# Performance work log

Hardware: AMD Instinct MI355X
Metric: run time of the kernel (lower is better)

## Reference

```python
import jax, jax.numpy as jnp
import numpy as np

N, C_IN, C_OUT, C_REL, T, V = 64, 256, 256, 32, 64, 25

def conv1x1(x, w, b):
    # x: (n, ci, a, b), w: (co, ci), b: (co,) -> (n, co, a, b)
    return jnp.einsum('oc,ncab->noab', w, x) + b[None, :, None, None]

def setup_inputs() -> dict:
    key = jax.random.key(0)
    ks = jax.random.split(key, 10)
    s_in = 1.0 / np.sqrt(C_IN)
    s_rel = 1.0 / np.sqrt(C_REL)
    return {
        'x': jax.random.normal(ks[0], (N, C_IN, T, V), dtype=jnp.float32),
        'A': jax.random.normal(ks[1], (V, V), dtype=jnp.float32),
        'w1': jax.random.uniform(ks[2], (C_REL, C_IN), jnp.float32, -s_in, s_in),
        'b1': jax.random.uniform(ks[3], (C_REL,), jnp.float32, -s_in, s_in),
        'w2': jax.random.uniform(ks[4], (C_REL, C_IN), jnp.float32, -s_in, s_in),
        'b2': jax.random.uniform(ks[5], (C_REL,), jnp.float32, -s_in, s_in),
        'w3': jax.random.uniform(ks[6], (C_OUT, C_IN), jnp.float32, -s_in, s_in),
        'b3': jax.random.uniform(ks[7], (C_OUT,), jnp.float32, -s_in, s_in),
        'w4': jax.random.uniform(ks[8], (C_OUT, C_REL), jnp.float32, -s_rel, s_rel),
        'b4': jax.random.uniform(ks[9], (C_OUT,), jnp.float32, -s_rel, s_rel),
        'threhold': 0,
        'alpha': 1,
    }

def reference(x, A, w1, b1, w2, b2, w3, b3, w4, b4, threhold, alpha):
    # x: (n, c, t, v)
    # pooled 1x1 convs: fold the T-mean before the channel mix (linear ops commute)
    xm = x.mean(-2)                                   # (n, c, v)
    x1 = jnp.einsum('oc,ncv->nov', w1, xm) + b1[None, :, None]   # (n, r, v)
    x2 = jnp.einsum('oc,ncv->nov', w2, xm) + b2[None, :, None]   # (n, r, v)
    x3 = conv1x1(x, w3, b3)                           # (n, co, t, v)
    # channel-wise affinity: outer difference + tanh -> (n, r, v, v)
    aff = jnp.tanh(x1[:, :, :, None] - x2[:, :, None, :])
    # 1x1 conv over rel channels, scale, add adjacency
    attn = jnp.einsum('or,nruv->nouv', w4, aff) + b4[None, :, None, None]
    attn = attn * alpha + A[None, None]               # (n, co, v, v)
    # graph conv contraction
    out = jnp.einsum('ncuv,nctu->nctv', attn, x3)     # (n, co, t, v)
    return out
```

## Files before the change

### kernel.cpp

```cpp
#include <hip/hip_runtime.h>

#define N_  64
#define CI  256
#define CO  256
#define CR  32
#define T_  64
#define V_  25
#define TV  (T_*V_)
#define VV  (V_*V_)
#define ATS 640

typedef __attribute__((ext_vector_type(8))) short bshort8;
typedef __attribute__((ext_vector_type(4))) float f32x4;

__device__ inline unsigned short f2bf(float f) {
    unsigned int u = __float_as_uint(f);
    return (unsigned short)((u + 0x7FFFu + ((u >> 16) & 1u)) >> 16);
}

__global__ __launch_bounds__(256) void k_mean_cvt(const float* __restrict__ x,
                                                  const float* __restrict__ w3,
                                                  const float* __restrict__ w4,
                                                  float* __restrict__ xm,
                                                  unsigned short* __restrict__ w3f,
                                                  unsigned short* __restrict__ w4f) {
    int b = blockIdx.x;
    if (b < 1600) {
        int idx = b * 256 + threadIdx.x;
        int v  = idx % V_;
        int nc = idx / V_;
        const float* p = x + (size_t)nc * TV + v;
        float s = 0.f;
        for (int t = 0; t < T_; ++t) s += p[t * V_];
        xm[idx] = s * (1.f / T_);
    } else if (b < 1632) {
        int f = (b - 1600) * 256 + threadIdx.x;
        int lane = f & 63;
        int ks = (f >> 6) & 7;
        int ot = f >> 9;
        const float* src = w3 + (size_t)(ot * 16 + (lane & 15)) * CI + ks * 32 + (lane >> 4) * 8;
        bshort8 v;
        #pragma unroll
        for (int i = 0; i < 8; ++i) v[i] = (short)f2bf(src[i]);
        *(bshort8*)(w3f + (size_t)f * 8) = v;
    } else {
        int f = (b - 1632) * 256 + threadIdx.x;
        int lane = f & 63;
        int ot = f >> 6;
        const float* src = w4 + (size_t)(ot * 16 + (lane & 15)) * CR + (lane >> 4) * 8;
        bshort8 v;
        #pragma unroll
        for (int i = 0; i < 8; ++i) v[i] = (short)f2bf(src[i]);
        *(bshort8*)(w4f + (size_t)f * 8) = v;
    }
}

__global__ __launch_bounds__(256) void k_x1x2(const float* __restrict__ xm,
                                              const float* __restrict__ w1,
                                              const float* __restrict__ b1,
                                              const float* __restrict__ w2,
                                              const float* __restrict__ b2,
                                              float* __restrict__ x1,
                                              float* __restrict__ x2) {
    int n = blockIdx.x, q = blockIdx.y;
    __shared__ float s_xm[CI * V_];
    const float4* src = (const float4*)(xm + (size_t)n * CI * V_);
    for (int i = threadIdx.x; i < CI * V_ / 4; i += 256) ((float4*)s_xm)[i] = src[i];
    __syncthreads();
    if (threadIdx.x < 200) {
        int idx = q * 200 + threadIdx.x;
        int r = idx / V_, v = idx % V_;
        const float* wr1 = w1 + (size_t)r * CI;
        const float* wr2 = w2 + (size_t)r * CI;
        float p1a = 0.f, p1b = 0.f, p2a = 0.f, p2b = 0.f;
        #pragma unroll 4
        for (int c = 0; c < CI; c += 2) {
            float xv0 = s_xm[c * V_ + v];
            float xv1 = s_xm[(c + 1) * V_ + v];
            p1a += wr1[c] * xv0;  p1b += wr1[c + 1] * xv1;
            p2a += wr2[c] * xv0;  p2b += wr2[c + 1] * xv1;
        }
        x1[n * CR * V_ + idx] = p1a + p1b + b1[r];
        x2[n * CR * V_ + idx] = p2a + p2b + b2[r];
    }
}

__global__ __launch_bounds__(256) void k_attn(const float* __restrict__ x1,
                                              const float* __restrict__ x2,
                                              const unsigned short* __restrict__ w4f,
                                              const float* __restrict__ b4,
                                              const float* __restrict__ A,
                                              const int* __restrict__ alpha_p,
                                              unsigned short* __restrict__ attnT) {
    int n = blockIdx.x;
    __shared__ float s_x1[CR * V_];
    __shared__ float s_x2[CR * V_];
    __shared__ float s_A[VV];
    int tid = threadIdx.x;
    float alpha = (float)alpha_p[0];
    for (int i = tid; i < CR * V_; i += 256) {
        s_x1[i] = x1[n * CR * V_ + i];
        s_x2[i] = x2[n * CR * V_ + i];
    }
    for (int i = tid; i < VV; i += 256) s_A[i] = A[i];
    __syncthreads();
    int wave = tid >> 6, lane = tid & 63;
    int task = blockIdx.y * 4 + wave;
    int og   = task & 3;
    int ug   = task >> 2;
    int o0   = og * 64;
    int quad = lane >> 4, c16 = lane & 15;
    bshort8 a[4];
    #pragma unroll
    for (int ot = 0; ot < 4; ++ot)
        a[ot] = *(const bshort8*)(w4f + (size_t)(((og * 4) + ot) * 64 + lane) * 8);
    float4 bv[4];
    #pragma unroll
    for (int ot = 0; ot < 4; ++ot)
        bv[ot] = *(const float4*)(b4 + o0 + ot * 16 + quad * 4);
    int r0 = quad * 8;
    #pragma unroll
    for (int it = 0; it < 5; ++it) {
        int uv0 = (ug * 5 + it) * 16;
        int uvc = uv0 + c16;
        bool valid = uvc < VV;
        int uvcc = valid ? uvc : (VV - 1);
        int u = uvcc % V_, v = uvcc / V_;
        bshort8 b;
        #pragma unroll
        for (int i = 0; i < 8; ++i) {
            float d = s_x1[(r0 + i) * V_ + u] - s_x2[(r0 + i) * V_ + v];
            b[i] = (short)f2bf(tanhf(d));
        }
        float Auv = s_A[u * V_ + v];
        f32x4 acc[4];
        #pragma unroll
        for (int ot = 0; ot < 4; ++ot)
            acc[ot] = __builtin_amdgcn_mfma_f32_16x16x32_bf16(a[ot], b, (f32x4){0,0,0,0}, 0, 0, 0);
        if (valid) {
            #pragma unroll
            for (int ot = 0; ot < 4; ++ot) {
                #pragma unroll
                for (int r = 0; r < 4; ++r) {
                    int o = o0 + ot * 16 + quad * 4 + r;
                    float bval = (r == 0) ? bv[ot].x : (r == 1) ? bv[ot].y
                               : (r == 2) ? bv[ot].z : bv[ot].w;
                    attnT[(size_t)(n * CO + o) * ATS + uvc] =
                        f2bf((acc[ot][r] + bval) * alpha + Auv);
                }
            }
        }
    }
}

__global__ __launch_bounds__(256) void k_gemm1(const float* __restrict__ x,
                                               const unsigned short* __restrict__ w3f,
                                               const float* __restrict__ b3,
                                               unsigned short* __restrict__ x3) {
    int n = blockIdx.x, j0 = blockIdx.y * 64;
    __shared__ unsigned short sB[64 * 256];
    int tid  = threadIdx.x;
    int lane = tid & 63, wave = tid >> 6;
    const float* gx = x + (size_t)n * CI * TV + j0;
    for (int i = 0; i < 16; ++i) {
        int task = i * 256 + tid;
        int c = task >> 4, chunk = task & 15;
        float4 v = *(const float4*)(gx + (size_t)c * TV + chunk * 4);
        int g0 = c >> 3, cl = c & 7;
        #pragma unroll
        for (int k = 0; k < 4; ++k) {
            int j = chunk * 4 + k;
            int f = g0 ^ (j & 7) ^ ((j >> 2) & 7);
            float val = (k == 0) ? v.x : (k == 1) ? v.y : (k == 2) ? v.z : v.w;
            sB[j * 256 + f * 8 + cl] = f2bf(val);
        }
    }
    __syncthreads();
    int quad = lane >> 4, c16 = lane & 15;
    const bshort8* Af = (const bshort8*)w3f;
    f32x4 acc[4][4];
    #pragma unroll
    for (int mt = 0; mt < 4; ++mt)
        #pragma unroll
        for (int nt = 0; nt < 4; ++nt) acc[mt][nt] = (f32x4){0,0,0,0};
    #pragma unroll
    for (int ks = 0; ks < 8; ++ks) {
        bshort8 b[4], a[4];
        #pragma unroll
        for (int nt = 0; nt < 4; ++nt) {
            int rB = nt * 16 + c16;
            int cidx = ks * 4 + quad;
            int f = cidx ^ (rB & 7) ^ ((rB >> 2) & 7);
            b[nt] = *(const bshort8*)(&sB[rB * 256 + f * 8]);
        }
        #pragma unroll
        for (int mt = 0; mt < 4; ++mt)
            a[mt] = Af[(size_t)(((wave * 4 + mt) * 8 + ks) * 64) + lane];
        #pragma unroll
        for (int mt = 0; mt < 4; ++mt)
            #pragma unroll
            for (int nt = 0; nt < 4; ++nt)
                acc[mt][nt] = __builtin_amdgcn_mfma_f32_16x16x32_bf16(a[mt], b[nt], acc[mt][nt], 0, 0, 0);
    }
    __syncthreads();
    unsigned short* eS = sB;
    #pragma unroll
    for (int pass = 0; pass < 2; ++pass) {
        if ((wave >> 1) == pass) {
            #pragma unroll
            for (int mt = 0; mt < 4; ++mt) {
                int o = wave * 64 + mt * 16 + quad * 4;
                float4 bvv = *(const float4*)(b3 + o);
                int ol = (wave & 1) * 64 + mt * 16 + quad * 4;
                #pragma unroll
                for (int nt = 0; nt < 4; ++nt) {
                    int jc = nt * 16 + c16;
                    eS[(ol + 0) * 72 + jc] = f2bf(acc[mt][nt][0] + bvv.x);
                    eS[(ol + 1) * 72 + jc] = f2bf(acc[mt][nt][1] + bvv.y);
                    eS[(ol + 2) * 72 + jc] = f2bf(acc[mt][nt][2] + bvv.z);
                    eS[(ol + 3) * 72 + jc] = f2bf(acc[mt][nt][3] + bvv.w);
                }
            }
        }
        __syncthreads();
        #pragma unroll
        for (int i = 0; i < 4; ++i) {
            int task = i * 256 + tid;
            int orow = task >> 3, seg = task & 7;
            bshort8 vv = *(const bshort8*)&eS[orow * 72 + seg * 8];
            *(bshort8*)(x3 + (size_t)(n * CO + pass * 128 + orow) * TV + j0 + seg * 8) = vv;
        }
        __syncthreads();
    }
}

__global__ __launch_bounds__(256) void k_contract(const unsigned short* __restrict__ x3,
                                                  const unsigned short* __restrict__ attnT,
                                                  float* __restrict__ out) {
    int no0 = blockIdx.x * 4;
    __shared__ __align__(16) unsigned char smem[28672];
    unsigned short* sA = (unsigned short*)smem;
    unsigned short* sB = (unsigned short*)(smem + 16384);
    float*          sO = (float*)smem;
    int tid = threadIdx.x;
    #pragma unroll
    for (int i = 0; i < 7; ++i) {
        int task = i * 256 + tid;
        if (task < 1792) {
            int p = task / 448, rem = task % 448;
            sA[p * 2048 + (rem / 7) * 32 + 25 + rem % 7] = 0;
        }
    }
    {
        int task = tid;
        for (int i = 0; i < 3; ++i, task += 256)
            if (task < 700) {
                int p = task / 175, rem = task % 175;
                sB[p * 1024 + (rem / 7) * 32 + 25 + rem % 7] = 0;
            }
    }
    #pragma unroll
    for (int i = 0; i < 4; ++i) {
        int task = i * 256 + tid;
        if (task < 800) {
            int p = task / 200, e8 = task % 200;
            bshort8 vv = *(const bshort8*)(x3 + (size_t)(no0 + p) * TV + e8 * 8);
            #pragma unroll
            for (int k = 0; k < 8; ++k) {
                int j = e8 * 8 + k;
                int t = j / 25, u = j % 25;
                sA[p * 2048 + t * 32 + u] = (unsigned short)vv[k];
            }
        }
    }
    #pragma unroll
    for (int i = 0; i < 2; ++i) {
        int task = i * 256 + tid;
        if (task < 316) {
            int p = task / 79, e8 = task % 79;
            bshort8 vv = *(const bshort8*)(attnT + (size_t)(no0 + p) * ATS + e8 * 8);
            #pragma unroll
            for (int k = 0; k < 8; ++k) {
                int idx = e8 * 8 + k;
                if (idx < VV) {
                    int v = idx / 25, u = idx % 25;
                    sB[p * 1024 + v * 32 + u] = (unsigned short)vv[k];
                }
            }
        }
    }
    __syncthreads();
    int p = tid >> 6, lane = tid & 63;
    int quad = lane >> 4, c16 = lane & 15;
    const unsigned short* pA = sA + p * 2048;
    const unsigned short* pB = sB + p * 1024;
    bshort8 a[4], b[2];
    #pragma unroll
    for (int mt = 0; mt < 4; ++mt) a[mt] = *(const bshort8*)&pA[(mt * 16 + c16) * 32 + quad * 8];
    #pragma unroll
    for (int nt = 0; nt < 2; ++nt) b[nt] = *(const bshort8*)&pB[(nt * 16 + c16) * 32 + quad * 8];
    f32x4 acc[4][2];
    #pragma unroll
    for (int mt = 0; mt < 4; ++mt)
        #pragma unroll
        for (int nt = 0; nt < 2; ++nt)
            acc[mt][nt] = __builtin_amdgcn_mfma_f32_16x16x32_bf16(a[mt], b[nt], (f32x4){0,0,0,0}, 0, 0, 0);
    __syncthreads();
    float* pO = sO + p * 1792;
    #pragma unroll
    for (int mt = 0; mt < 4; ++mt)
        #pragma unroll
        for (int nt = 0; nt < 2; ++nt) {
            int v = nt * 16 + c16;
            if (v < V_) {
                #pragma unroll
                for (int r = 0; r < 4; ++r) {
                    int t = mt * 16 + quad * 4 + r;
                    pO[t * 28 + v] = acc[mt][nt][r];
                }
            }
        }
    __syncthreads();
    #pragma unroll
    for (int i = 0; i < 25; ++i) {
        int idx = i * 256 + tid;
        int p2 = idx / TV, rem = idx % TV;
        int t = rem / 25, v = rem % 25;
        out[(size_t)(no0 + p2) * TV + rem] = sO[p2 * 1792 + t * 28 + v];
    }
}

extern "C" void kernel_launch(void* const* d_in, const int* in_sizes, int n_in,
                              void* d_out, int out_size, void* d_ws, size_t ws_size,
                              hipStream_t stream) {
    const float* x  = (const float*)d_in[0];
    const float* A  = (const float*)d_in[1];
    const float* w1 = (const float*)d_in[2];
    const float* b1 = (const float*)d_in[3];
    const float* w2 = (const float*)d_in[4];
    const float* b2 = (const float*)d_in[5];
    const float* w3 = (const float*)d_in[6];
    const float* b3 = (const float*)d_in[7];
    const float* w4 = (const float*)d_in[8];
    const float* b4 = (const float*)d_in[9];
    const int* alpha_p = (const int*)d_in[11];
    float* out = (float*)d_out;

    float* ws = (float*)d_ws;
    float* xm = ws;
    float* x1 = ws + 409600;
    float* x2 = ws + 460800;
    unsigned short* attnT = (unsigned short*)(ws + 512000);
    unsigned short* w3f   = attnT + (size_t)16384 * ATS;
    unsigned short* w4f   = w3f + 65536;
    unsigned short* x3    = w4f + 16384;

    k_mean_cvt<<<1636, 256, 0, stream>>>(x, w3, w4, xm, w3f, w4f);
    k_x1x2<<<dim3(N_, 4), 256, 0, stream>>>(xm, w1, b1, w2, b2, x1, x2);
    k_attn<<<dim3(N_, 8), 256, 0, stream>>>(x1, x2, w4f, b4, A, alpha_p, attnT);
    k_gemm1<<<dim3(N_, 25), 256, 0, stream>>>(x, w3f, b3, x3);
    k_contract<<<4096, 256, 0, stream>>>(x3, attnT, out);
}
```

Measured before the change: 297.9 us.

## Merge attention and GEMM kernels, tile T-mean via LDS, write contract output directly

Three changes. The T-mean reduction now stages 16-channel tiles of x through shared memory with float4 loads instead of strided scalar loads per (n,c,v). The attention-build and x3 GEMM kernels are combined into one launch with block-index dispatch, which removes a launch and lets the small attention work overlap the GEMM. The contraction kernel drops its shared-memory staging and writes results straight to global memory, giving up coalescing in exchange for fewer barriers and less LDS. The fused kernel now uses 64KB of static LDS for every block, including the attention blocks, which may lower occupancy.

```diff
diff --git a/kernel.cpp b/kernel.cpp
--- a/kernel.cpp
+++ b/kernel.cpp
@@ -25,16 +25,43 @@
                                                   unsigned short* __restrict__ w3f,
                                                   unsigned short* __restrict__ w4f) {
     int b = blockIdx.x;
-    if (b < 1600) {
-        int idx = b * 256 + threadIdx.x;
-        int v  = idx % V_;
-        int nc = idx / V_;
-        const float* p = x + (size_t)nc * TV + v;
-        float s = 0.f;
-        for (int t = 0; t < T_; ++t) s += p[t * V_];
-        xm[idx] = s * (1.f / T_);
-    } else if (b < 1632) {
-        int f = (b - 1600) * 256 + threadIdx.x;
+    int tid = threadIdx.x;
+    if (b < 1024) {
+        __shared__ float L[16 * 400];
+        int n = b >> 4, c0 = (b & 15) * 16;
+        float a0 = 0.f, a1 = 0.f;
+        for (int ch = 0; ch < 4; ++ch) {
+            for (int i = 0; i < 7; ++i) {
+                int task = i * 256 + tid;
+                if (task < 1600) {
+                    int c = task / 100, f4 = task % 100;
+                    *(float4*)&L[c * 400 + f4 * 4] =
+                        *(const float4*)(x + (size_t)(n * CI + c0 + c) * TV + ch * 400 + f4 * 4);
+                }
+            }
+            __syncthreads();
+            {
+                int c = tid / 25, v = tid % 25;
+                float s = 0.f;
+                #pragma unroll
+                for (int tl = 0; tl < 16; ++tl) s += L[c * 400 + tl * 25 + v];
+                a0 += s;
+            }
+            if (tid < 144) {
+                int oi = tid + 256;
+                int c = oi / 25, v = oi % 25;
+                float s = 0.f;
+                #pragma unroll
+                for (int tl = 0; tl < 16; ++tl) s += L[c * 400 + tl * 25 + v];
+                a1 += s;
+            }
+            __syncthreads();
+        }
+        xm[(size_t)(n * CI + c0) * V_ + tid] = a0 * (1.f / T_);
+        if (tid < 144)
+            xm[(size_t)(n * CI + c0) * V_ + tid + 256] = a1 * (1.f / T_);
+    } else if (b < 1056) {
+        int f = (b - 1024) * 256 + tid;
         int lane = f & 63;
         int ks = (f >> 6) & 7;
         int ot = f >> 9;
@@ -44,7 +71,7 @@
         for (int i = 0; i < 8; ++i) v[i] = (short)f2bf(src[i]);
         *(bshort8*)(w3f + (size_t)f * 8) = v;
     } else {
-        int f = (b - 1632) * 256 + threadIdx.x;
+        int f = (b - 1056) * 256 + tid;
         int lane = f & 63;
         int ot = f >> 6;
         const float* src = w4 + (size_t)(ot * 16 + (lane & 15)) * CR + (lane >> 4) * 8;
@@ -85,152 +112,155 @@
     }
 }
 
-__global__ __launch_bounds__(256) void k_attn(const float* __restrict__ x1,
-                                              const float* __restrict__ x2,
-                                              const unsigned short* __restrict__ w4f,
-                                              const float* __restrict__ b4,
-                                              const float* __restrict__ A,
-                                              const int* __restrict__ alpha_p,
-                                              unsigned short* __restrict__ attnT) {
-    int n = blockIdx.x;
-    __shared__ float s_x1[CR * V_];
-    __shared__ float s_x2[CR * V_];
-    __shared__ float s_A[VV];
+__global__ __launch_bounds__(256) void k_attn_gemm(const float* __restrict__ x,
+                                                   const unsigned short* __restrict__ w3f,
+                                                   const float* __restrict__ b3,
+                                                   unsigned short* __restrict__ x3,
+                                                   const float* __restrict__ x1,
+                                                   const float* __restrict__ x2,
+                                                   const unsigned short* __restrict__ w4f,
+                                                   const float* __restrict__ b4,
+                                                   const float* __restrict__ A,
+                                                   const int* __restrict__ alpha_p,
+                                                   unsigned short* __restrict__ attnT) {
+    __shared__ __align__(16) unsigned char smem[65536];
     int tid = threadIdx.x;
-    float alpha = (float)alpha_p[0];
-    for (int i = tid; i < CR * V_; i += 256) {
-        s_x1[i] = x1[n * CR * V_ + i];
-        s_x2[i] = x2[n * CR * V_ + i];
-    }
-    for (int i = tid; i < VV; i += 256) s_A[i] = A[i];
-    __syncthreads();
-    int wave = tid >> 6, lane = tid & 63;
-    int task = blockIdx.y * 4 + wave;
-    int og   = task & 3;
-    int ug   = task >> 2;
-    int o0   = og * 64;
-    int quad = lane >> 4, c16 = lane & 15;
-    bshort8 a[4];
-    #pragma unroll
-    for (int ot = 0; ot < 4; ++ot)
-        a[ot] = *(const bshort8*)(w4f + (size_t)(((og * 4) + ot) * 64 + lane) * 8);
-    float4 bv[4];
-    #pragma unroll
-    for (int ot = 0; ot < 4; ++ot)
-        bv[ot] = *(const float4*)(b4 + o0 + ot * 16 + quad * 4);
-    int r0 = quad * 8;
-    #pragma unroll
-    for (int it = 0; it < 5; ++it) {
-        int uv0 = (ug * 5 + it) * 16;
-        int uvc = uv0 + c16;
-        bool valid = uvc < VV;
-        int uvcc = valid ? uvc : (VV - 1);
-        int u = uvcc % V_, v = uvcc / V_;
-        bshort8 b;
-        #pragma unroll
-        for (int i = 0; i < 8; ++i) {
-            float d = s_x1[(r0 + i) * V_ + u] - s_x2[(r0 + i) * V_ + v];
-            b[i] = (short)f2bf(tanhf(d));
-        }
-        float Auv = s_A[u * V_ + v];
-        f32x4 acc[4];
+    int bb  = blockIdx.x;
+    if (bb < 1600) {
+        unsigned short* sB = (unsigned short*)smem;
+        int n = bb / 25, j0 = (bb % 25) * 64;
+        int lane = tid & 63, wave = tid >> 6;
+        const float* gx = x + (size_t)n * CI * TV + j0;
+        for (int i = 0; i < 16; ++i) {
+            int task = i * 256 + tid;
+            int c = task >> 4, chunk = task & 15;
+            float4 v = *(const float4*)(gx + (size_t)c * TV + chunk * 4);
+            int g0 = c >> 3, cl = c & 7;
+            #pragma unroll
+            for (int k = 0; k < 4; ++k) {
+                int j = chunk * 4 + k;
+                int f = g0 ^ (j & 7) ^ ((j >> 2) & 7);
+                float val = (k == 0) ? v.x : (k == 1) ? v.y : (k == 2) ? v.z : v.w;
+                sB[j * 256 + f * 8 + cl] = f2bf(val);
+            }
+        }
+        __syncthreads();
+        int quad = lane >> 4, c16 = lane & 15;
+        const bshort8* Af = (const bshort8*)w3f;
+        f32x4 acc[4][4];
+        #pragma unroll
+        for (int mt = 0; mt < 4; ++mt)
+            #pragma unroll
+            for (int nt = 0; nt < 4; ++nt) acc[mt][nt] = (f32x4){0,0,0,0};
+        #pragma unroll
+        for (int ks = 0; ks < 8; ++ks) {
+            bshort8 b[4], a[4];
+            #pragma unroll
+            for (int nt = 0; nt < 4; ++nt) {
+                int rB = nt * 16 + c16;
+                int cidx = ks * 4 + quad;
+                int f = cidx ^ (rB & 7) ^ ((rB >> 2) & 7);
+                b[nt] = *(const bshort8*)(&sB[rB * 256 + f * 8]);
+            }
+            #pragma unroll
+            for (int mt = 0; mt < 4; ++mt)
+                a[mt] = Af[(size_t)(((wave * 4 + mt) * 8 + ks) * 64) + lane];
+            #pragma unroll
+            for (int mt = 0; mt < 4; ++mt)
+                #pragma unroll
+                for (int nt = 0; nt < 4; ++nt)
+                    acc[mt][nt] = __builtin_amdgcn_mfma_f32_16x16x32_bf16(a[mt], b[nt], acc[mt][nt], 0, 0, 0);
+        }
+        __syncthreads();
+        unsigned short* eS = sB;
+        #pragma unroll
+        for (int pass = 0; pass < 2; ++pass) {
+            if ((wave >> 1) == pass) {
+                #pragma unroll
+                for (int mt = 0; mt < 4; ++mt) {
+                    int o = wave * 64 + mt * 16 + quad * 4;
+                    float4 bvv = *(const float4*)(b3 + o);
+                    int ol = (wave & 1) * 64 + mt * 16 + quad * 4;
+                    #pragma unroll
+                    for (int nt = 0; nt < 4; ++nt) {
+                        int jc = nt * 16 + c16;
+                        eS[(ol + 0) * 72 + jc] = f2bf(acc[mt][nt][0] + bvv.x);
+                        eS[(ol + 1) * 72 + jc] = f2bf(acc[mt][nt][1] + bvv.y);
+                        eS[(ol + 2) * 72 + jc] = f2bf(acc[mt][nt][2] + bvv.z);
+                        eS[(ol + 3) * 72 + jc] = f2bf(acc[mt][nt][3] + bvv.w);
+                    }
+                }
+            }
+            __syncthreads();
+            #pragma unroll
+            for (int i = 0; i < 4; ++i) {
+                int task = i * 256 + tid;
+                int orow = task >> 3, seg = task & 7;
+                bshort8 vv = *(const bshort8*)&eS[orow * 72 + seg * 8];
+                *(bshort8*)(x3 + (size_t)(n * CO + pass * 128 + orow) * TV + j0 + seg * 8) = vv;
+            }
+            __syncthreads();
+        }
+    } else {
+        float* s_x1 = (float*)smem;
+        float* s_x2 = s_x1 + CR * V_;
+        float* s_A  = s_x2 + CR * V_;
+        int b2 = bb - 1600;
+        int n = b2 >> 3, by = b2 & 7;
+        float alpha = (float)alpha_p[0];
+        for (int i = tid; i < CR * V_; i += 256) {
+            s_x1[i] = x1[n * CR * V_ + i];
+            s_x2[i] = x2[n * CR * V_ + i];
+        }
+        for (int i = tid; i < VV; i += 256) s_A[i] = A[i];
+        __syncthreads();
+        int wave = tid >> 6, lane = tid & 63;
+        int task = by * 4 + wave;
+        int og   = task & 3;
+        int ug   = task >> 2;
+        int o0   = og * 64;
+        int quad = lane >> 4, c16 = lane & 15;
+        bshort8 a[4];
         #pragma unroll
         for (int ot = 0; ot < 4; ++ot)
-            acc[ot] = __builtin_amdgcn_mfma_f32_16x16x32_bf16(a[ot], b, (f32x4){0,0,0,0}, 0, 0, 0);
-        if (valid) {
-            #pragma unroll
-            for (int ot = 0; ot < 4; ++ot) {
-                #pragma unroll
-                for (int r = 0; r < 4; ++r) {
-                    int o = o0 + ot * 16 + quad * 4 + r;
-                    float bval = (r == 0) ? bv[ot].x : (r == 1) ? bv[ot].y
-                               : (r == 2) ? bv[ot].z : bv[ot].w;
-                    attnT[(size_t)(n * CO + o) * ATS + uvc] =
-                        f2bf((acc[ot][r] + bval) * alpha + Auv);
-                }
-            }
-        }
-    }
-}
-
-__global__ __launch_bounds__(256) void k_gemm1(const float* __restrict__ x,
-                                               const unsigned short* __restrict__ w3f,
-                                               const float* __restrict__ b3,
-                                               unsigned short* __restrict__ x3) {
-    int n = blockIdx.x, j0 = blockIdx.y * 64;
-    __shared__ unsigned short sB[64 * 256];
-    int tid  = threadIdx.x;
-    int lane = tid & 63, wave = tid >> 6;
-    const float* gx = x + (size_t)n * CI * TV + j0;
-    for (int i = 0; i < 16; ++i) {
-        int task = i * 256 + tid;
-        int c = task >> 4, chunk = task & 15;
-        float4 v = *(const float4*)(gx + (size_t)c * TV + chunk * 4);
-        int g0 = c >> 3, cl = c & 7;
-        #pragma unroll
-        for (int k = 0; k < 4; ++k) {
-            int j = chunk * 4 + k;
-            int f = g0 ^ (j & 7) ^ ((j >> 2) & 7);
-            float val = (k == 0) ? v.x : (k == 1) ? v.y : (k == 2) ? v.z : v.w;
-            sB[j * 256 + f * 8 + cl] = f2bf(val);
-        }
-    }
-    __syncthreads();
-    int quad = lane >> 4, c16 = lane & 15;
-    const bshort8* Af = (const bshort8*)w3f;
-    f32x4 acc[4][4];
-    #pragma unroll
-    for (int mt = 0; mt < 4; ++mt)
-        #pragma unroll
-        for (int nt = 0; nt < 4; ++nt) acc[mt][nt] = (f32x4){0,0,0,0};
-    #pragma unroll
-    for (int ks = 0; ks < 8; ++ks) {
-        bshort8 b[4], a[4];
-        #pragma unroll
-        for (int nt = 0; nt < 4; ++nt) {
-            int rB = nt * 16 + c16;
-            int cidx = ks * 4 + quad;
-            int f = cidx ^ (rB & 7) ^ ((rB >> 2) & 7);
-            b[nt] = *(const bshort8*)(&sB[rB * 256 + f * 8]);
-        }
-        #pragma unroll
-        for (int mt = 0; mt < 4; ++mt)
-            a[mt] = Af[(size_t)(((wave * 4 + mt) * 8 + ks) * 64) + lane];
-        #pragma unroll
-        for (int mt = 0; mt < 4; ++mt)
-            #pragma unroll
-            for (int nt = 0; nt < 4; ++nt)
-                acc[mt][nt] = __builtin_amdgcn_mfma_f32_16x16x32_bf16(a[mt], b[nt], acc[mt][nt], 0, 0, 0);
-    }
-    __syncthreads();
-    unsigned short* eS = sB;
-    #pragma unroll
-    for (int pass = 0; pass < 2; ++pass) {
-        if ((wave >> 1) == pass) {
-            #pragma unroll
-            for (int mt = 0; mt < 4; ++mt) {
-                int o = wave * 64 + mt * 16 + quad * 4;
-                float4 bvv = *(const float4*)(b3 + o);
-                int ol = (wave & 1) * 64 + mt * 16 + quad * 4;
-                #pragma unroll
-                for (int nt = 0; nt < 4; ++nt) {
-                    int jc = nt * 16 + c16;
-                    eS[(ol + 0) * 72 + jc] = f2bf(acc[mt][nt][0] + bvv.x);
-                    eS[(ol + 1) * 72 + jc] = f2bf(acc[mt][nt][1] + bvv.y);
-                    eS[(ol + 2) * 72 + jc] = f2bf(acc[mt][nt][2] + bvv.z);
-                    eS[(ol + 3) * 72 + jc] = f2bf(acc[mt][nt][3] + bvv.w);
-                }
-            }
-        }
-        __syncthreads();
-        #pragma unroll
-        for (int i = 0; i < 4; ++i) {
-            int task = i * 256 + tid;
-            int orow = task >> 3, seg = task & 7;
-            bshort8 vv = *(const bshort8*)&eS[orow * 72 + seg * 8];
-            *(bshort8*)(x3 + (size_t)(n * CO + pass * 128 + orow) * TV + j0 + seg * 8) = vv;
-        }
-        __syncthreads();
+            a[ot] = *(const bshort8*)(w4f + (size_t)(((og * 4) + ot) * 64 + lane) * 8);
+        float4 bv[4];
+        #pragma unroll
+        for (int ot = 0; ot < 4; ++ot)
+            bv[ot] = *(const float4*)(b4 + o0 + ot * 16 + quad * 4);
+        int r0 = quad * 8;
+        #pragma unroll
+        for (int it = 0; it < 5; ++it) {
+            int uv0 = (ug * 5 + it) * 16;
+            int uvc = uv0 + c16;
+            bool valid = uvc < VV;
+            int uvcc = valid ? uvc : (VV - 1);
+            int u = uvcc % V_, v = uvcc / V_;
+            bshort8 b;
+            #pragma unroll
+            for (int i = 0; i < 8; ++i) {
+                float d = s_x1[(r0 + i) * V_ + u] - s_x2[(r0 + i) * V_ + v];
+                b[i] = (short)f2bf(tanhf(d));
+            }
+            float Auv = s_A[u * V_ + v];
+            f32x4 acc[4];
+            #pragma unroll
+            for (int ot = 0; ot < 4; ++ot)
+                acc[ot] = __builtin_amdgcn_mfma_f32_16x16x32_bf16(a[ot], b, (f32x4){0,0,0,0}, 0, 0, 0);
+            if (valid) {
+                #pragma unroll
+                for (int ot = 0; ot < 4; ++ot) {
+                    #pragma unroll
+                    for (int r = 0; r < 4; ++r) {
+                        int o = o0 + ot * 16 + quad * 4 + r;
+                        float bval = (r == 0) ? bv[ot].x : (r == 1) ? bv[ot].y
+                                   : (r == 2) ? bv[ot].z : bv[ot].w;
+                        attnT[(size_t)(n * CO + o) * ATS + uvc] =
+                            f2bf((acc[ot][r] + bval) * alpha + Auv);
+                    }
+                }
+            }
+        }
     }
 }
 
@@ -238,10 +268,9 @@
                                                   const unsigned short* __restrict__ attnT,
                                                   float* __restrict__ out) {
     int no0 = blockIdx.x * 4;
-    __shared__ __align__(16) unsigned char smem[28672];
+    __shared__ __align__(16) unsigned char smem[24576];
     unsigned short* sA = (unsigned short*)smem;
     unsigned short* sB = (unsigned short*)(smem + 16384);
-    float*          sO = (float*)smem;
     int tid = threadIdx.x;
     #pragma unroll
     for (int i = 0; i < 7; ++i) {
@@ -305,8 +334,7 @@
         #pragma unroll
         for (int nt = 0; nt < 2; ++nt)
             acc[mt][nt] = __builtin_amdgcn_mfma_f32_16x16x32_bf16(a[mt], b[nt], (f32x4){0,0,0,0}, 0, 0, 0);
-    __syncthreads();
-    float* pO = sO + p * 1792;
+    size_t ob = (size_t)(no0 + p) * TV;
     #pragma unroll
     for (int mt = 0; mt < 4; ++mt)
         #pragma unroll
@@ -316,18 +344,10 @@
                 #pragma unroll
                 for (int r = 0; r < 4; ++r) {
                     int t = mt * 16 + quad * 4 + r;
-                    pO[t * 28 + v] = acc[mt][nt][r];
-                }
-            }
-        }
-    __syncthreads();
-    #pragma unroll
-    for (int i = 0; i < 25; ++i) {
-        int idx = i * 256 + tid;
-        int p2 = idx / TV, rem = idx % TV;
-        int t = rem / 25, v = rem % 25;
-        out[(size_t)(no0 + p2) * TV + rem] = sO[p2 * 1792 + t * 28 + v];
-    }
+                    out[ob + t * 25 + v] = acc[mt][nt][r];
+                }
+            }
+        }
 }
 
 extern "C" void kernel_launch(void* const* d_in, const int* in_sizes, int n_in,
@@ -355,9 +375,8 @@
     unsigned short* w4f   = w3f + 65536;
     unsigned short* x3    = w4f + 16384;
 
-    k_mean_cvt<<<1636, 256, 0, stream>>>(x, w3, w4, xm, w3f, w4f);
+    k_mean_cvt<<<1060, 256, 0, stream>>>(x, w3, w4, xm, w3f, w4f);
     k_x1x2<<<dim3(N_, 4), 256, 0, stream>>>(xm, w1, b1, w2, b2, x1, x2);
-    k_attn<<<dim3(N_, 8), 256, 0, stream>>>(x1, x2, w4f, b4, A, alpha_p, attnT);
-    k_gemm1<<<dim3(N_, 25), 256, 0, stream>>>(x, w3f, b3, x3);
+    k_attn_gemm<<<2112, 256, 0, stream>>>(x, w3f, b3, x3, x1, x2, w4f, b4, A, alpha_p, attnT);
     k_contract<<<4096, 256, 0, stream>>>(x3, attnT, out);
 }
```

New measurement: 295.9 us. Within noise of the previous version (-0.7%).
